# Kernel optimization log

Measured on AMD Instinct MI355X. Metric: run time of the kernel, lower is better.

The kernel has to match this reference:

```python
import jax, jax.numpy as jnp
import numpy as np

B, C, CI = 4, 1024, 512
T, H, W = 16, 28, 28
STD = 0.01  # init std used by the torch module
BN_EPS = 1e-5


def _conv1x1(x, w, b):
    # x: (B,C,T,H,W), w: (O,C), b: (O,)
    return jnp.einsum('bcthw,oc->bothw', x, w) + b[None, :, None, None, None]


def _maxpool2(x):
    # 3D max pool, kernel=stride=2 over (T,H,W)
    b, c, t, h, w = x.shape
    x = x.reshape(b, c, t // 2, 2, h // 2, 2, w // 2, 2)
    return x.max(axis=(3, 5, 7))


def setup_inputs() -> dict:
    key = jax.random.key(0)
    ks = jax.random.split(key, 6)
    return {
        'x': jax.random.normal(ks[0], (B, C, T, H, W), jnp.float32),
        'g_w': STD * jax.random.normal(ks[1], (CI, C), jnp.float32),
        'g_b': jnp.zeros((CI,), jnp.float32),
        'theta_w': STD * jax.random.normal(ks[2], (CI, C), jnp.float32),
        'theta_b': jnp.zeros((CI,), jnp.float32),
        'phi_w': STD * jax.random.normal(ks[3], (CI, C), jnp.float32),
        'phi_b': jnp.zeros((CI,), jnp.float32),
        'w_w': STD * jax.random.normal(ks[4], (C, CI), jnp.float32),
        'w_b': jnp.zeros((C,), jnp.float32),
        'bn_gamma': STD * jax.random.normal(ks[5], (C,), jnp.float32),
        'bn_beta': jnp.zeros((C,), jnp.float32),
    }


def reference(x, g_w, g_b, theta_w, theta_b, phi_w, phi_b, w_w, w_b, bn_gamma, bn_beta):
    b = x.shape[0]
    # g and phi branches are sub-sampled by maxpool(2)
    g_x = _maxpool2(_conv1x1(x, g_w, g_b)).reshape(b, CI, -1)          # (B,Ci,M)
    g_x = g_x.transpose(0, 2, 1)                                        # (B,M,Ci)
    theta_x = _conv1x1(x, theta_w, theta_b).reshape(b, CI, -1)          # (B,Ci,N)
    theta_x = theta_x.transpose(0, 2, 1)                                # (B,N,Ci)
    phi_x = _maxpool2(_conv1x1(x, phi_w, phi_b)).reshape(b, CI, -1)     # (B,Ci,M)
    # embedded gaussian: softmax(theta @ phi) @ g  (unscaled)
    f = jnp.einsum('bnc,bcm->bnm', theta_x, phi_x)                      # (B,N,M)
    f_div_C = jax.nn.softmax(f, axis=-1)
    y = jnp.einsum('bnm,bmc->bnc', f_div_C, g_x)                        # (B,N,Ci)
    y = y.transpose(0, 2, 1).reshape(b, CI, *x.shape[2:])               # (B,Ci,T,H,W)
    # W: 1x1 conv + BatchNorm (eval mode: running_mean=0, running_var=1)
    w_y = _conv1x1(y, w_w, w_b)
    scale = bn_gamma / jnp.sqrt(jnp.float32(1.0) + BN_EPS)
    w_y = w_y * scale[None, :, None, None, None] + bn_beta[None, :, None, None, None]
    return w_y + x
```

## Files before the change

kernel.cpp:

```cpp
#include <hip/hip_runtime.h>

#define DEVI __device__ __forceinline__

typedef __bf16 bf16x8 __attribute__((ext_vector_type(8)));
typedef float f32x4 __attribute__((ext_vector_type(4)));
typedef unsigned short u16;
typedef long long i64;

constexpr int B_ = 4;
constexpr int C_ = 1024;
constexpr int CI_ = 512;
constexpr int C3_ = 3 * CI_;
constexpr int N_ = 16 * 28 * 28;
constexpr int M_ = 8 * 14 * 14;
constexpr int MP_ = 1792;

DEVI u16 f2bf(float f) { __bf16 b = (__bf16)f; return __builtin_bit_cast(u16, b); }
DEVI float bf2f(u16 u) { return (float)__builtin_bit_cast(__bf16, u); }

#define GLOBAL_AS __attribute__((address_space(1)))
#define LDS_AS __attribute__((address_space(3)))

DEVI void load16(const u16* g, u16* l) {
  __builtin_amdgcn_global_load_lds((const GLOBAL_AS void*)g, (LDS_AS void*)l, 16, 0, 0);
}

#define SYNC_V(N)                                        \
  asm volatile("s_waitcnt vmcnt(" #N ")" ::: "memory");  \
  __builtin_amdgcn_s_barrier();                          \
  asm volatile("" ::: "memory");

template <int MODE>
__global__ __launch_bounds__(512, 2)
void gemm_tn(const u16* __restrict__ A, const u16* __restrict__ Bm,
             void* __restrict__ Cp, int K, int lda, int ldb, int ldc,
             i64 sA, i64 sB, i64 sC,
             const float* __restrict__ e0, const float* __restrict__ e1,
             const float* __restrict__ e2, const float* __restrict__ xres, i64 sX) {
  __shared__ u16 sm[2 * 32768];
  const int b = blockIdx.z;
  A += (size_t)b * sA;
  Bm += (size_t)b * sB;
  const size_t cbase = (size_t)b * sC;
  if constexpr (MODE == 3) xres += (size_t)b * sX;

  const int tid = threadIdx.x;
  const int lane = tid & 63;
  const int wave = tid >> 6;
  const int wm = wave >> 2;
  const int wn = wave & 3;
  const int i0 = blockIdx.y * 256;
  const int j0 = blockIdx.x * 256;

  const int rs = tid >> 2;
  const int swz = ((tid & 3) ^ ((rs >> 1) & 3)) * 8;
  const u16* Ag0 = A + (size_t)(i0 + rs) * lda + swz;
  const u16* Bg0 = Bm + (size_t)(j0 + rs) * ldb + swz;
  const i64 ldA128 = (i64)128 * lda;
  const i64 ldB128 = (i64)128 * ldb;
  u16* ldsT = sm + tid * 8;

  auto stA = [&](int buf, int kh, int k0) {
    const u16* s = Ag0 + k0 + kh * 32;
    u16* d = ldsT + buf * 32768 + kh * 8192;
    load16(s, d);
    load16(s + ldA128, d + 4096);
  };
  auto stB = [&](int buf, int kh, int k0) {
    const u16* s = Bg0 + k0 + kh * 32;
    u16* d = ldsT + buf * 32768 + 16384 + kh * 8192;
    load16(s, d);
    load16(s + ldB128, d + 4096);
  };

  const int l15 = lane & 15;
  const int slR = (((lane >> 4) ^ ((l15 >> 1) & 3)) * 8);
  const int arow = wm * 128 + l15;
  const int brow = wn * 64 + l15;

  f32x4 acc[8][4] = {};

#define KHALF(BUF, KH, S1, S2, SYNC)                                           \
  {                                                                            \
    const u16* Ab_ = sm + (BUF) * 32768 + (KH) * 8192;                         \
    const u16* Bb_ = Ab_ + 16384;                                              \
    bf16x8 bv[4], a0[4], a1[4];                                                \
    _Pragma("unroll") for (int n = 0; n < 4; ++n)                              \
        bv[n] = *(const bf16x8*)&Bb_[(brow + n * 16) * 32 + slR];              \
    _Pragma("unroll") for (int f = 0; f < 4; ++f)                              \
        a0[f] = *(const bf16x8*)&Ab_[(arow + f * 16) * 32 + slR];              \
    S1;                                                                        \
    __builtin_amdgcn_s_setprio(1);                                             \
    _Pragma("unroll") for (int f = 0; f < 4; ++f)                              \
        _Pragma("unroll") for (int n = 0; n < 4; ++n)                          \
            acc[f][n] = __builtin_amdgcn_mfma_f32_16x16x32_bf16(               \
                a0[f], bv[n], acc[f][n], 0, 0, 0);                             \
    __builtin_amdgcn_s_setprio(0);                                             \
    _Pragma("unroll") for (int f = 0; f < 4; ++f)                              \
        a1[f] = *(const bf16x8*)&Ab_[(arow + (f + 4) * 16) * 32 + slR];        \
    S2;                                                                        \
    __builtin_amdgcn_s_setprio(1);                                             \
    _Pragma("unroll") for (int f = 0; f < 4; ++f)                              \
        _Pragma("unroll") for (int n = 0; n < 4; ++n)                          \
            acc[f + 4][n] = __builtin_amdgcn_mfma_f32_16x16x32_bf16(           \
                a1[f], bv[n], acc[f + 4][n], 0, 0, 0);                         \
    __builtin_amdgcn_s_setprio(0);                                             \
    SYNC                                                                       \
  }

  const int NT = K >> 6;

  stA(0, 0, 0); stB(0, 0, 0);
  stA(0, 1, 0); stB(0, 1, 0);
  stA(1, 0, 64); stB(1, 0, 64);
  SYNC_V(8);

  for (int t = 0; t < NT - 2; ++t) {
    const int bc = t & 1;
    const int k0 = t * 64;
    KHALF(bc, 0, stA(bc ^ 1, 1, k0 + 64), stB(bc ^ 1, 1, k0 + 64), SYNC_V(8));
    KHALF(bc, 1, stA(bc, 0, k0 + 128), stB(bc, 0, k0 + 128), SYNC_V(8));
  }
  {
    const int bc = (NT - 2) & 1;
    stA(bc ^ 1, 1, (NT - 1) * 64);
    stB(bc ^ 1, 1, (NT - 1) * 64);
    SYNC_V(0);
    KHALF(bc, 0, (void)0, (void)0, );
    KHALF(bc, 1, (void)0, (void)0, );
    KHALF(bc ^ 1, 0, (void)0, (void)0, );
    KHALF(bc ^ 1, 1, (void)0, (void)0, );
  }
#undef KHALF

  const int rr0 = i0 + wm * 128 + ((lane >> 4) << 2);
  const int cc0 = j0 + wn * 64 + (lane & 15);
  float* Cf = (float*)Cp;
  u16* Cs = (u16*)Cp;
#pragma unroll
  for (int mi = 0; mi < 8; ++mi) {
#pragma unroll
    for (int ni = 0; ni < 4; ++ni) {
      const int col = cc0 + ni * 16;
#pragma unroll
      for (int r = 0; r < 4; ++r) {
        const int row = rr0 + mi * 16 + r;
        const size_t idx = cbase + (size_t)row * ldc + col;
        float v = acc[mi][ni][r];
        if constexpr (MODE == 0) {
          Cs[idx] = f2bf(v + e0[col]);
        } else if constexpr (MODE == 1) {
          Cs[idx] = f2bf(v);
        } else {
          const float sc = e1[row] * rsqrtf(1.0f + 1e-5f);
          Cf[idx] = (v + e0[row]) * sc + e2[row] + xres[(size_t)row * ldc + col];
        }
      }
    }
  }
}

__global__ __launch_bounds__(256)
void transpose_cast_x(const float* __restrict__ src, u16* __restrict__ dst) {
  __shared__ u16 tile[32][33];
  const size_t so = (size_t)blockIdx.z * C_ * N_;
  const int n0 = blockIdx.x * 32;
  const int c0 = blockIdx.y * 32;
  const int tx = threadIdx.x & 31;
  const int ty = threadIdx.x >> 5;
#pragma unroll
  for (int rr = 0; rr < 32; rr += 8)
    tile[ty + rr][tx] = f2bf(src[so + (size_t)(c0 + ty + rr) * N_ + n0 + tx]);
  __syncthreads();
#pragma unroll
  for (int rr = 0; rr < 32; rr += 8)
    dst[so + (size_t)(n0 + ty + rr) * C_ + c0 + tx] = tile[tx][ty + rr];
}

__global__ __launch_bounds__(256)
void transpose_bf16(const u16* __restrict__ src, u16* __restrict__ dst) {
  __shared__ u16 tile[32][33];
  const int b = blockIdx.z;
  const int c0 = blockIdx.x * 32;
  const int r0 = blockIdx.y * 32;
  const int tx = threadIdx.x & 31;
  const int ty = threadIdx.x >> 5;
#pragma unroll
  for (int rr = 0; rr < 32; rr += 8)
    tile[ty + rr][tx] = src[(size_t)b * MP_ * CI_ + (size_t)(r0 + ty + rr) * CI_ + c0 + tx];
  __syncthreads();
#pragma unroll
  for (int rr = 0; rr < 32; rr += 8)
    dst[(size_t)b * CI_ * MP_ + (size_t)(c0 + ty + rr) * MP_ + r0 + tx] = tile[tx][ty + rr];
}

__global__ __launch_bounds__(256)
void cast_weights(const float* s0, const float* s1, const float* s2, const float* s3,
                  u16* d0, u16* d1, u16* d2, u16* d3) {
  const int idx = blockIdx.x * 256 + threadIdx.x;
  const float* s;
  u16* d;
  switch (blockIdx.y) {
    case 0: s = s0; d = d0; break;
    case 1: s = s1; d = d1; break;
    case 2: s = s2; d = d2; break;
    default: s = s3; d = d3; break;
  }
  d[idx] = f2bf(s[idx]);
}

__global__ __launch_bounds__(256)
void concat_bias(const float* tb, const float* gb, const float* pb, float* dst) {
  const int i = blockIdx.x * 256 + threadIdx.x;
  if (i >= C3_) return;
  dst[i] = (i < CI_) ? tb[i] : (i < 2 * CI_) ? gb[i - CI_] : pb[i - 2 * CI_];
}

__global__ __launch_bounds__(256)
void pool2(const u16* __restrict__ CO, u16* __restrict__ Gp, u16* __restrict__ Pp) {
  const int b = blockIdx.z;
  const int which = blockIdx.y;
  const u16* src = CO + (size_t)b * N_ * C3_ + CI_ + which * CI_;
  u16* dst = (which ? Pp : Gp) + (size_t)b * MP_ * CI_;
  const int idx = blockIdx.x * 256 + threadIdx.x;
  const int m = idx >> 9;
  const int ci = idx & 511;
  if (m >= M_) { dst[idx] = 0; return; }
  const int t = m / 196, r = m % 196, h = r / 14, w = r % 14;
  const int nb = 2 * t * 784 + 2 * h * 28 + 2 * w;
  float mx = -1e30f;
#pragma unroll
  for (int dt = 0; dt < 2; ++dt)
#pragma unroll
    for (int dh = 0; dh < 2; ++dh)
#pragma unroll
      for (int dw = 0; dw < 2; ++dw)
        mx = fmaxf(mx, bf2f(src[(size_t)(nb + dt * 784 + dh * 28 + dw) * C3_ + ci]));
  dst[idx] = f2bf(mx);
}

__global__ __launch_bounds__(256)
void softmax_k(u16* __restrict__ F) {
  u16* row = F + ((size_t)blockIdx.y * N_ + blockIdx.x) * MP_;
  const int tid = threadIdx.x;
  float v[7];
  float mx = -1e30f;
#pragma unroll
  for (int it = 0; it < 7; ++it) {
    const int j = tid + it * 256;
    v[it] = (j < M_) ? bf2f(row[j]) : -1e30f;
    mx = fmaxf(mx, v[it]);
  }
#pragma unroll
  for (int off = 32; off >= 1; off >>= 1) mx = fmaxf(mx, __shfl_xor(mx, off));
  __shared__ float redm[4], reds[4];
  const int wv = tid >> 6;
  if ((tid & 63) == 0) redm[wv] = mx;
  __syncthreads();
  mx = fmaxf(fmaxf(redm[0], redm[1]), fmaxf(redm[2], redm[3]));
  float s = 0.f;
#pragma unroll
  for (int it = 0; it < 7; ++it) {
    const int j = tid + it * 256;
    v[it] = (j < M_) ? __expf(v[it] - mx) : 0.f;
    s += v[it];
  }
#pragma unroll
  for (int off = 32; off >= 1; off >>= 1) s += __shfl_xor(s, off);
  if ((tid & 63) == 0) reds[wv] = s;
  __syncthreads();
  s = reds[0] + reds[1] + reds[2] + reds[3];
  const float inv = 1.f / s;
#pragma unroll
  for (int it = 0; it < 7; ++it) {
    const int j = tid + it * 256;
    if (j < MP_) row[j] = f2bf(v[it] * inv);
  }
}

extern "C" void kernel_launch(void* const* d_in, const int* in_sizes, int n_in,
                              void* d_out, int out_size, void* d_ws, size_t ws_size,
                              hipStream_t stream) {
  (void)in_sizes; (void)n_in; (void)out_size;
  const float* x    = (const float*)d_in[0];
  const float* g_w  = (const float*)d_in[1];
  const float* g_b  = (const float*)d_in[2];
  const float* th_w = (const float*)d_in[3];
  const float* th_b = (const float*)d_in[4];
  const float* ph_w = (const float*)d_in[5];
  const float* ph_b = (const float*)d_in[6];
  const float* w_w  = (const float*)d_in[7];
  const float* w_b  = (const float*)d_in[8];
  const float* bn_g = (const float*)d_in[9];
  const float* bn_b = (const float*)d_in[10];
  float* out = (float*)d_out;

  auto align256 = [](size_t b) { return (b + 255) & ~(size_t)255; };
  const size_t fixed_bytes = align256((size_t)C3_ * C_ * 2) + align256((size_t)C_ * CI_ * 2) +
                             align256((size_t)C3_ * 4);
  const size_t per_batch = align256((size_t)N_ * C_ * 2)
                         + align256((size_t)N_ * C3_ * 2)
                         + align256((size_t)N_ * MP_ * 2)
                         + align256((size_t)N_ * CI_ * 2)
                         + 3 * align256((size_t)MP_ * CI_ * 2);
  int G = 4;
  while (G > 1 && fixed_bytes + (size_t)G * per_batch > ws_size) G >>= 1;

  char* ws = (char*)d_ws;
  size_t off = 0;
  auto alloc = [&](size_t bytes) -> void* {
    void* p = ws + off;
    off += align256(bytes);
    return p;
  };
  u16* wcat = (u16*)alloc((size_t)C3_ * C_ * 2);
  u16* wwB  = (u16*)alloc((size_t)C_ * CI_ * 2);
  float* eb = (float*)alloc((size_t)C3_ * 4);
  u16* Xt  = (u16*)alloc((size_t)G * N_ * C_ * 2);
  u16* CO  = (u16*)alloc((size_t)G * N_ * C3_ * 2);
  u16* Fb  = (u16*)alloc((size_t)G * N_ * MP_ * 2);
  u16* Yb  = (u16*)alloc((size_t)G * N_ * CI_ * 2);
  u16* Gp  = (u16*)alloc((size_t)G * MP_ * CI_ * 2);
  u16* Pp  = (u16*)alloc((size_t)G * MP_ * CI_ * 2);
  u16* Gp2 = (u16*)alloc((size_t)G * CI_ * MP_ * 2);

  const dim3 blk(256);
  const dim3 gblk(512);
  cast_weights<<<dim3(2048, 4), blk, 0, stream>>>(
      th_w, g_w, ph_w, w_w, wcat, wcat + (size_t)CI_ * C_, wcat + (size_t)2 * CI_ * C_, wwB);
  concat_bias<<<dim3(6), blk, 0, stream>>>(th_b, g_b, ph_b, eb);

  for (int bg = 0; bg < B_; bg += G) {
    const float* xg = x + (size_t)bg * C_ * N_;
    float* og = out + (size_t)bg * C_ * N_;
    transpose_cast_x<<<dim3(N_ / 32, C_ / 32, G), blk, 0, stream>>>(xg, Xt);
    gemm_tn<0><<<dim3(C3_ / 256, G * N_ / 256, 1), gblk, 0, stream>>>(
        Xt, wcat, CO, C_, C_, C_, C3_, 0, 0, 0, eb, nullptr, nullptr, nullptr, 0);
    pool2<<<dim3(MP_ * CI_ / 256, 2, G), blk, 0, stream>>>(CO, Gp, Pp);
    transpose_bf16<<<dim3(CI_ / 32, MP_ / 32, G), blk, 0, stream>>>(Gp, Gp2);
    gemm_tn<1><<<dim3(MP_ / 256, N_ / 256, G), gblk, 0, stream>>>(
        CO, Pp, Fb, CI_, C3_, CI_, MP_,
        (i64)N_ * C3_, (i64)MP_ * CI_, (i64)N_ * MP_, nullptr, nullptr, nullptr, nullptr, 0);
    softmax_k<<<dim3(N_, G), blk, 0, stream>>>(Fb);
    gemm_tn<1><<<dim3(CI_ / 256, N_ / 256, G), gblk, 0, stream>>>(
        Fb, Gp2, Yb, MP_, MP_, MP_, CI_,
        (i64)N_ * MP_, (i64)CI_ * MP_, (i64)N_ * CI_, nullptr, nullptr, nullptr, nullptr, 0);
    gemm_tn<3><<<dim3(N_ / 256, C_ / 256, G), gblk, 0, stream>>>(
        wwB, Yb, og, CI_, CI_, CI_, N_,
        0, (i64)N_ * CI_, (i64)C_ * N_, w_b, bn_g, bn_b, xg, (i64)C_ * N_);
  }
}
```

Before: 1.014 ms.

## Remap GEMM blocks across XCDs, restructure LDS pipeline, vectorize softmax rows

```diff
diff --git a/kernel.cpp b/kernel.cpp
--- a/kernel.cpp
+++ b/kernel.cpp
@@ -5,6 +5,7 @@
 typedef __bf16 bf16x8 __attribute__((ext_vector_type(8)));
 typedef float f32x4 __attribute__((ext_vector_type(4)));
 typedef unsigned short u16;
+typedef u16 u16x8v __attribute__((ext_vector_type(8)));
 typedef long long i64;
 
 constexpr int B_ = 4;
@@ -28,7 +29,7 @@
 #define SYNC_V(N)                                        \
   asm volatile("s_waitcnt vmcnt(" #N ")" ::: "memory");  \
   __builtin_amdgcn_s_barrier();                          \
-  asm volatile("" ::: "memory");
+  __builtin_amdgcn_sched_barrier(0);
 
 template <int MODE>
 __global__ __launch_bounds__(512, 2)
@@ -44,13 +45,22 @@
   const size_t cbase = (size_t)b * sC;
   if constexpr (MODE == 3) xres += (size_t)b * sX;
 
+  const int gx = gridDim.x;
+  const int nwg = gx * gridDim.y;
+  int flat = blockIdx.y * gx + blockIdx.x;
+  {
+    const int q = nwg >> 3, r = nwg & 7;
+    const int xcd = flat & 7, sidx = flat >> 3;
+    flat = (xcd < r ? xcd * (q + 1) : r * (q + 1) + (xcd - r) * q) + sidx;
+  }
+  const int i0 = (flat / gx) * 256;
+  const int j0 = (flat % gx) * 256;
+
   const int tid = threadIdx.x;
   const int lane = tid & 63;
   const int wave = tid >> 6;
   const int wm = wave >> 2;
   const int wn = wave & 3;
-  const int i0 = blockIdx.y * 256;
-  const int j0 = blockIdx.x * 256;
 
   const int rs = tid >> 2;
   const int swz = ((tid & 3) ^ ((rs >> 1) & 3)) * 8;
@@ -80,7 +90,7 @@
 
   f32x4 acc[8][4] = {};
 
-#define KHALF(BUF, KH, S1, S2, SYNC)                                           \
+#define KHALF(BUF, KH, STG, SYNC)                                              \
   {                                                                            \
     const u16* Ab_ = sm + (BUF) * 32768 + (KH) * 8192;                         \
     const u16* Bb_ = Ab_ + 16384;                                              \
@@ -89,23 +99,20 @@
         bv[n] = *(const bf16x8*)&Bb_[(brow + n * 16) * 32 + slR];              \
     _Pragma("unroll") for (int f = 0; f < 4; ++f)                              \
         a0[f] = *(const bf16x8*)&Ab_[(arow + f * 16) * 32 + slR];              \
-    S1;                                                                        \
+    _Pragma("unroll") for (int f = 0; f < 4; ++f)                              \
+        a1[f] = *(const bf16x8*)&Ab_[(arow + (f + 4) * 16) * 32 + slR];        \
+    STG;                                                                       \
+    SYNC                                                                       \
     __builtin_amdgcn_s_setprio(1);                                             \
     _Pragma("unroll") for (int f = 0; f < 4; ++f)                              \
         _Pragma("unroll") for (int n = 0; n < 4; ++n)                          \
             acc[f][n] = __builtin_amdgcn_mfma_f32_16x16x32_bf16(               \
                 a0[f], bv[n], acc[f][n], 0, 0, 0);                             \
-    __builtin_amdgcn_s_setprio(0);                                             \
-    _Pragma("unroll") for (int f = 0; f < 4; ++f)                              \
-        a1[f] = *(const bf16x8*)&Ab_[(arow + (f + 4) * 16) * 32 + slR];        \
-    S2;                                                                        \
-    __builtin_amdgcn_s_setprio(1);                                             \
     _Pragma("unroll") for (int f = 0; f < 4; ++f)                              \
         _Pragma("unroll") for (int n = 0; n < 4; ++n)                          \
             acc[f + 4][n] = __builtin_amdgcn_mfma_f32_16x16x32_bf16(           \
                 a1[f], bv[n], acc[f + 4][n], 0, 0, 0);                         \
     __builtin_amdgcn_s_setprio(0);                                             \
-    SYNC                                                                       \
   }
 
   const int NT = K >> 6;
@@ -118,18 +125,15 @@
   for (int t = 0; t < NT - 2; ++t) {
     const int bc = t & 1;
     const int k0 = t * 64;
-    KHALF(bc, 0, stA(bc ^ 1, 1, k0 + 64), stB(bc ^ 1, 1, k0 + 64), SYNC_V(8));
-    KHALF(bc, 1, stA(bc, 0, k0 + 128), stB(bc, 0, k0 + 128), SYNC_V(8));
+    KHALF(bc, 0, { stA(bc ^ 1, 1, k0 + 64); stB(bc ^ 1, 1, k0 + 64); }, SYNC_V(8));
+    KHALF(bc, 1, { stA(bc, 0, k0 + 128); stB(bc, 0, k0 + 128); }, SYNC_V(8));
   }
   {
     const int bc = (NT - 2) & 1;
-    stA(bc ^ 1, 1, (NT - 1) * 64);
-    stB(bc ^ 1, 1, (NT - 1) * 64);
-    SYNC_V(0);
-    KHALF(bc, 0, (void)0, (void)0, );
-    KHALF(bc, 1, (void)0, (void)0, );
-    KHALF(bc ^ 1, 0, (void)0, (void)0, );
-    KHALF(bc ^ 1, 1, (void)0, (void)0, );
+    KHALF(bc, 0, { stA(bc ^ 1, 1, (NT - 1) * 64); stB(bc ^ 1, 1, (NT - 1) * 64); }, SYNC_V(8));
+    KHALF(bc, 1, { (void)0; }, SYNC_V(4));
+    KHALF(bc ^ 1, 0, { (void)0; }, SYNC_V(0));
+    KHALF(bc ^ 1, 1, { (void)0; }, );
   }
 #undef KHALF
 
@@ -243,13 +247,13 @@
 void softmax_k(u16* __restrict__ F) {
   u16* row = F + ((size_t)blockIdx.y * N_ + blockIdx.x) * MP_;
   const int tid = threadIdx.x;
-  float v[7];
+  const bool valid = tid < 196;
+  float v[8];
   float mx = -1e30f;
-#pragma unroll
-  for (int it = 0; it < 7; ++it) {
-    const int j = tid + it * 256;
-    v[it] = (j < M_) ? bf2f(row[j]) : -1e30f;
-    mx = fmaxf(mx, v[it]);
+  if (valid) {
+    u16x8v pk = *(const u16x8v*)&row[tid * 8];
+#pragma unroll
+    for (int i = 0; i < 8; ++i) { v[i] = bf2f(pk[i]); mx = fmaxf(mx, v[i]); }
   }
 #pragma unroll
   for (int off = 32; off >= 1; off >>= 1) mx = fmaxf(mx, __shfl_xor(mx, off));
@@ -259,22 +263,20 @@
   __syncthreads();
   mx = fmaxf(fmaxf(redm[0], redm[1]), fmaxf(redm[2], redm[3]));
   float s = 0.f;
-#pragma unroll
-  for (int it = 0; it < 7; ++it) {
-    const int j = tid + it * 256;
-    v[it] = (j < M_) ? __expf(v[it] - mx) : 0.f;
-    s += v[it];
+  if (valid) {
+#pragma unroll
+    for (int i = 0; i < 8; ++i) { v[i] = __expf(v[i] - mx); s += v[i]; }
   }
 #pragma unroll
   for (int off = 32; off >= 1; off >>= 1) s += __shfl_xor(s, off);
   if ((tid & 63) == 0) reds[wv] = s;
   __syncthreads();
-  s = reds[0] + reds[1] + reds[2] + reds[3];
-  const float inv = 1.f / s;
-#pragma unroll
-  for (int it = 0; it < 7; ++it) {
-    const int j = tid + it * 256;
-    if (j < MP_) row[j] = f2bf(v[it] * inv);
+  const float inv = 1.f / (reds[0] + reds[1] + reds[2] + reds[3]);
+  if (valid) {
+    u16x8v pk;
+#pragma unroll
+    for (int i = 0; i < 8; ++i) pk[i] = f2bf(v[i] * inv);
+    *(u16x8v*)&row[tid * 8] = pk;
   }
 }
 
```

After: 992.0 us. -2.2%, faster.
